# Optimization experiments

Hardware: AMD Instinct MI355X
Metric: run time of the kernel (lower is better)

## Reference

```python
import jax, jax.numpy as jnp
import numpy as np

DIM = 1024
HEADS = 16
HEAD_DIM = DIM // HEADS
EPS = 1e-6

def _layernorm(x, gamma, beta):
    # LayerNorm over last axis (head_dim), biased variance like torch
    mu = jnp.mean(x, axis=-1, keepdims=True)
    var = jnp.mean(jnp.square(x - mu), axis=-1, keepdims=True)
    return (x - mu) * jax.lax.rsqrt(var + EPS) * gamma + beta

def setup_inputs() -> dict:
    key = jax.random.key(0)
    ks = jax.random.split(key, 12)
    B, N, D = 2, 2048, DIM
    s = 1.0 / np.sqrt(D)
    inp = {
        'x': jax.random.normal(ks[0], (B, N, D), jnp.float32),
        'attn_bias': jax.random.normal(ks[1], (B, 1, N, N), jnp.float32),
        'Wq': jax.random.normal(ks[2], (D, D), jnp.float32) * s,
        'bq': jnp.zeros((D,), jnp.float32),
        'Wk': jax.random.normal(ks[3], (D, D), jnp.float32) * s,
        'bk': jnp.zeros((D,), jnp.float32),
        'Wv': jax.random.normal(ks[4], (D, D), jnp.float32) * s,
        'bv': jnp.zeros((D,), jnp.float32),
        'Wo': jax.random.normal(ks[5], (D, D), jnp.float32) * s,
        'bo': jnp.zeros((D,), jnp.float32),
        'q_gamma': jnp.ones((HEAD_DIM,), jnp.float32),
        'q_beta': jnp.zeros((HEAD_DIM,), jnp.float32),
        'k_gamma': jnp.ones((HEAD_DIM,), jnp.float32),
        'k_beta': jnp.zeros((HEAD_DIM,), jnp.float32),
    }
    return inp

def reference(x, attn_bias, Wq, bq, Wk, bk, Wv, bv, Wo, bo, q_gamma, q_beta, k_gamma, k_beta):
    B, N, D = x.shape
    h, dh = HEADS, HEAD_DIM
    # QKV projections (torch Linear: x @ W.T + b) -> (B, h, N, dh)
    def proj(W, b):
        y = jnp.einsum('bnd,ed->bne', x, W) + b
        return y.reshape(B, N, h, dh).transpose(0, 2, 1, 3)
    q = proj(Wq, bq)
    k = proj(Wk, bk)
    v = proj(Wv, bv)
    # per-head LayerNorm on Q and K
    q = _layernorm(q, q_gamma, q_beta)
    k = _layernorm(k, k_gamma, k_beta)
    # scaled dot-product attention with additive graph bias
    scores = jnp.einsum('bhnd,bhmd->bhnm', q, k) / np.sqrt(dh).astype(np.float32)
    scores = scores + attn_bias  # (B,1,N,N) broadcasts over heads
    attn = jax.nn.softmax(scores, axis=-1)
    out = jnp.einsum('bhnm,bhmd->bhnd', attn, v)
    out = out.transpose(0, 2, 1, 3).reshape(B, N, D)
    return jnp.einsum('bnd,ed->bne', out, Wo) + bo
```

## Files before the change

kernel.cpp:

```cpp
#include <hip/hip_runtime.h>
#include <hip/hip_bf16.h>
#include <hip/hip_fp16.h>

#define D_MODEL 1024
#define N_SEQ   2048
#define N_B     2
#define M_ROWS  (N_B * N_SEQ)

typedef __attribute__((ext_vector_type(8))) short bf16x8;
typedef __attribute__((ext_vector_type(4))) float f32x4;

typedef const __attribute__((address_space(1))) unsigned int gu32_t;
typedef __attribute__((address_space(3))) unsigned int lu32_t;

__device__ __forceinline__ void gload16(const void* g, void* l) {
  __builtin_amdgcn_global_load_lds((gu32_t*)g, (lu32_t*)l, 16, 0, 0);
}

__device__ inline unsigned short f2bf(float f) {
  union { float f; unsigned int u; } v; v.f = f;
  unsigned int r = (v.u + 0x7FFFu + ((v.u >> 16) & 1u)) >> 16;
  return (unsigned short)r;
}

__device__ __forceinline__ unsigned int cvt_pk_bf16(float a, float b) {
  unsigned int r;
  asm("v_cvt_pk_bf16_f32 %0, %1, %2" : "=v"(r) : "v"(a), "v"(b));
  return r;
}

__device__ __forceinline__ float exp2fast(float x) {
#if __has_builtin(__builtin_amdgcn_exp2f)
  return __builtin_amdgcn_exp2f(x);
#else
  return __expf(x * 0.69314718056f);
#endif
}

#define WAITV(N) asm volatile("s_waitcnt vmcnt(" #N ")" ::: "memory")

__device__ __forceinline__ int lds_off(int row, int col ) {
  return row * 64 + (((col >> 3) ^ (row & 7)) << 3) + (col & 7);
}

template<int ROWS, int NTHR = 256>
__device__ __forceinline__ void stage_tile(const unsigned short* gbase, size_t gstride,
                                           unsigned short* lds, int tid) {
  const int wave = tid >> 6;
#pragma unroll
  for (int rnd = 0; rnd < ROWS * 8 / NTHR; ++rnd) {
    int c = rnd * NTHR + tid;
    int row = c >> 3, pc = c & 7;
    int gcol = ((pc ^ (row & 7)) << 3);
    gload16(gbase + (size_t)row * gstride + gcol,
            lds + (size_t)(rnd * NTHR + wave * 64) * 8);
  }
}

__device__ __forceinline__ void stage_bias(const unsigned short* gbase,
                                           unsigned short* lds, int tid) {
  const int wave = tid >> 6;
#pragma unroll
  for (int rnd = 0; rnd < 2; ++rnd) {
    int c = rnd * 512 + tid;
    int row = c >> 3, pc = c & 7;
    gload16(gbase + (size_t)row * N_SEQ + pc * 8,
            lds + (size_t)(rnd * 512 + wave * 64) * 8);
  }
}

constexpr size_t XEL = (size_t)M_ROWS * D_MODEL;
constexpr size_t WEL = (size_t)D_MODEL * D_MODEL;
constexpr size_t BEL = (size_t)N_B * N_SEQ * N_SEQ;
constexpr size_t TOTEL = XEL + 4 * WEL + BEL;

__launch_bounds__(256)
__global__ void cvt_kernel(const float* __restrict__ x, const float* __restrict__ bias,
                           const float* __restrict__ wq, const float* __restrict__ wk,
                           const float* __restrict__ wv, const float* __restrict__ wo,
                           unsigned short* __restrict__ dst,
                           unsigned short* __restrict__ dstB) {
  size_t i = ((size_t)blockIdx.x * 256 + threadIdx.x) * 8;
  if (i >= TOTEL) return;
  if (i >= XEL + 4 * WEL) {
    size_t off = i - (XEL + 4 * WEL);
    int row = (int)(off >> 11);
    int key = (int)(off & 2047);
    constexpr float LOG2E = 1.44269504088896340736f;
    float4 f0 = *(const float4*)(bias + off);
    float4 f1 = *(const float4*)(bias + off + 4);
    __half t[8] = { __float2half(f0.x * LOG2E), __float2half(f0.y * LOG2E),
                    __float2half(f0.z * LOG2E), __float2half(f0.w * LOG2E),
                    __float2half(f1.x * LOG2E), __float2half(f1.y * LOG2E),
                    __float2half(f1.z * LOG2E), __float2half(f1.w * LOG2E) };
    int j  = (key >> 3) & 7;
    int jp = j ^ ((row >> 1) & 7);
    uint4 v = *(const uint4*)t;
    if (row & 1) { uint4 w; w.x = v.z; w.y = v.w; w.z = v.x; w.w = v.y; v = w; }
    *(uint4*)(dstB + (((size_t)row << 11) + (key & ~63) + jp * 8)) = v;
    return;
  }
  const float* s; size_t off = i;
  if (off < XEL)                { s = x; }
  else if (off < XEL + WEL)     { s = wq; off -= XEL; }
  else if (off < XEL + 2*WEL)   { s = wk; off -= XEL + WEL; }
  else if (off < XEL + 3*WEL)   { s = wv; off -= XEL + 2*WEL; }
  else                          { s = wo; off -= XEL + 3*WEL; }
  float4 f0 = *(const float4*)(s + off);
  float4 f1 = *(const float4*)(s + off + 4);
  unsigned short t[8] = { f2bf(f0.x), f2bf(f0.y), f2bf(f0.z), f2bf(f0.w),
                          f2bf(f1.x), f2bf(f1.y), f2bf(f1.z), f2bf(f1.w) };
  *(uint4*)(dst + i) = *(const uint4*)t;
}

__device__ __forceinline__ void mainloop128(const unsigned short* __restrict__ A,
                                            const unsigned short* __restrict__ Bw,
                                            int m0, int e0,
                                            unsigned short* As, unsigned short* Bs,
                                            f32x4 (&acc)[4][4]) {
  const int tid  = threadIdx.x;
  const int wave = tid >> 6, lane = tid & 63;
  const int l16 = lane & 15, quad = lane >> 4;
  const int wr = wave >> 1, wc = wave & 1;

  for (int kt = 0; kt < D_MODEL / 64; ++kt) {
    const int k0 = kt * 64;
    stage_tile<128>(A + (size_t)m0 * D_MODEL + k0, D_MODEL, As, tid);
    stage_tile<128>(Bw + (size_t)e0 * D_MODEL + k0, D_MODEL, Bs, tid);
    __syncthreads();
#pragma unroll
    for (int ks = 0; ks < 2; ++ks) {
      bf16x8 af[4], bfr[4];
#pragma unroll
      for (int mi = 0; mi < 4; ++mi)
        af[mi] = *(const bf16x8*)(As + lds_off(wr * 64 + mi * 16 + l16, ks * 32 + quad * 8));
#pragma unroll
      for (int ci = 0; ci < 4; ++ci)
        bfr[ci] = *(const bf16x8*)(Bs + lds_off(wc * 64 + ci * 16 + l16, ks * 32 + quad * 8));
#pragma unroll
      for (int mi = 0; mi < 4; ++mi)
#pragma unroll
        for (int ci = 0; ci < 4; ++ci)
          acc[mi][ci] = __builtin_amdgcn_mfma_f32_16x16x32_bf16(af[mi], bfr[ci], acc[mi][ci], 0, 0, 0);
    }
    __syncthreads();
  }
}

__launch_bounds__(256)
__global__ void qkv_gemm(const unsigned short* __restrict__ xb,
                         const unsigned short* __restrict__ wb,
                         const float* __restrict__ bq, const float* __restrict__ bk,
                         const float* __restrict__ bv,
                         const float* __restrict__ qg, const float* __restrict__ qbeta,
                         const float* __restrict__ kg, const float* __restrict__ kbeta,
                         unsigned short* __restrict__ qkout,
                         unsigned short* __restrict__ vt) {
  __shared__ unsigned short As[128 * 64];
  __shared__ unsigned short Bs[128 * 64];
  const int m0  = blockIdx.x * 128;
  const int by  = blockIdx.y;
  const int mat = by >> 3;
  const int e0  = (by & 7) * 128;
  const unsigned short* Bw = wb + (size_t)mat * WEL;

  f32x4 acc[4][4];
#pragma unroll
  for (int mi = 0; mi < 4; ++mi)
#pragma unroll
    for (int ci = 0; ci < 4; ++ci) acc[mi][ci] = f32x4{0.f, 0.f, 0.f, 0.f};

  mainloop128(xb, Bw, m0, e0, As, Bs, acc);

  const int lane = threadIdx.x & 63, wave = threadIdx.x >> 6;
  const int l16 = lane & 15, quad = lane >> 4;
  const int wr = wave >> 1, wc = wave & 1;
  const int colbase = e0 + wc * 64;

  const float* bias = (mat == 0) ? bq : ((mat == 1) ? bk : bv);
  float bcol[4];
#pragma unroll
  for (int ci = 0; ci < 4; ++ci) bcol[ci] = bias[colbase + ci * 16 + l16];
#pragma unroll
  for (int mi = 0; mi < 4; ++mi)
#pragma unroll
    for (int ci = 0; ci < 4; ++ci)
#pragma unroll
      for (int r = 0; r < 4; ++r) acc[mi][ci][r] += bcol[ci];

  if (mat < 2) {
    const float* gamma = (mat == 0) ? qg : kg;
    const float* beta  = (mat == 0) ? qbeta : kbeta;
    const float sc = (mat == 0) ? 0.18033688011112042f : 1.0f;
    float g4[4], bt4[4];
#pragma unroll
    for (int ci = 0; ci < 4; ++ci) {
      g4[ci] = gamma[ci * 16 + l16] * sc;
      bt4[ci] = beta[ci * 16 + l16] * sc;
    }
#pragma unroll
    for (int mi = 0; mi < 4; ++mi)
#pragma unroll
      for (int r = 0; r < 4; ++r) {
        float s = acc[mi][0][r] + acc[mi][1][r] + acc[mi][2][r] + acc[mi][3][r];
        s += __shfl_xor(s, 1); s += __shfl_xor(s, 2);
        s += __shfl_xor(s, 4); s += __shfl_xor(s, 8);
        float mean = s * (1.f / 64.f);
        float d0 = acc[mi][0][r] - mean, d1 = acc[mi][1][r] - mean;
        float d2 = acc[mi][2][r] - mean, d3 = acc[mi][3][r] - mean;
        float q = d0 * d0 + d1 * d1 + d2 * d2 + d3 * d3;
        q += __shfl_xor(q, 1); q += __shfl_xor(q, 2);
        q += __shfl_xor(q, 4); q += __shfl_xor(q, 8);
        float rs = rsqrtf(q * (1.f / 64.f) + 1e-6f);
        acc[mi][0][r] = d0 * rs * g4[0] + bt4[0];
        acc[mi][1][r] = d1 * rs * g4[1] + bt4[1];
        acc[mi][2][r] = d2 * rs * g4[2] + bt4[2];
        acc[mi][3][r] = d3 * rs * g4[3] + bt4[3];
      }
    unsigned short* out = qkout + (size_t)mat * XEL;
#pragma unroll
    for (int mi = 0; mi < 4; ++mi)
#pragma unroll
      for (int ci = 0; ci < 4; ++ci) {
        int col = colbase + ci * 16 + l16;
#pragma unroll
        for (int r = 0; r < 4; ++r) {
          int row = m0 + wr * 64 + mi * 16 + quad * 4 + r;
          out[(size_t)row * D_MODEL + col] = f2bf(acc[mi][ci][r]);
        }
      }
  } else {
    unsigned short* scr = ((wave < 2) ? As : Bs) + (size_t)(wave & 1) * 4096;
#pragma unroll
    for (int ci = 0; ci < 4; ++ci) {
      int dl = ci * 16 + l16;
      int sw = (dl & 3) * 16;
#pragma unroll
      for (int mi = 0; mi < 4; ++mi)
#pragma unroll
        for (int r = 0; r < 4; ++r) {
          int np = ((mi >> 1) << 5) + (quad << 3) + ((mi & 1) << 2) + r;
          scr[dl * 64 + (np ^ sw)] = f2bf(acc[mi][ci][r]);
        }
    }
    __builtin_amdgcn_wave_barrier();
    int row0 = m0 + wr * 64;
    int b = row0 >> 11, nb = row0 & 2047;
    int h = colbase >> 6;
    int dl = lane;
    unsigned short* gdst = vt + ((size_t)((b * 16 + h) * 64 + dl) * N_SEQ + nb);
    const unsigned short* srow = scr + dl * 64;
    int sw = (dl & 3) * 16;
#pragma unroll
    for (int j = 0; j < 8; ++j) {
      uint4 vv = *(const uint4*)(srow + ((j * 8) ^ sw));
      *(uint4*)(gdst + j * 8) = vv;
    }
  }
}

__launch_bounds__(256)
__global__ void out_gemm(const unsigned short* __restrict__ ao,
                         const unsigned short* __restrict__ wob,
                         const float* __restrict__ bo,
                         float* __restrict__ out) {
  __shared__ unsigned short As[128 * 64];
  __shared__ unsigned short Bs[128 * 64];
  const int m0 = blockIdx.x * 128;
  const int e0 = blockIdx.y * 128;

  f32x4 acc[4][4];
#pragma unroll
  for (int mi = 0; mi < 4; ++mi)
#pragma unroll
    for (int ci = 0; ci < 4; ++ci) acc[mi][ci] = f32x4{0.f, 0.f, 0.f, 0.f};

  mainloop128(ao, wob, m0, e0, As, Bs, acc);

  const int lane = threadIdx.x & 63, wave = threadIdx.x >> 6;
  const int l16 = lane & 15, quad = lane >> 4;
  const int wr = wave >> 1, wc = wave & 1;
  float bcol[4];
#pragma unroll
  for (int ci = 0; ci < 4; ++ci) bcol[ci] = bo[e0 + wc * 64 + ci * 16 + l16];
#pragma unroll
  for (int mi = 0; mi < 4; ++mi)
#pragma unroll
    for (int ci = 0; ci < 4; ++ci) {
      int col = e0 + wc * 64 + ci * 16 + l16;
#pragma unroll
      for (int r = 0; r < 4; ++r) {
        int row = m0 + wr * 64 + mi * 16 + quad * 4 + r;
        out[(size_t)row * D_MODEL + col] = acc[mi][ci][r] + bcol[ci];
      }
    }
}

__launch_bounds__(512, 4)
__global__ void attn_kernel(const unsigned short* __restrict__ Q,
                            const unsigned short* __restrict__ Kn,
                            const unsigned short* __restrict__ Vt,
                            const unsigned short* __restrict__ bias16,
                            unsigned short* __restrict__ Out) {
  __shared__ unsigned short smem[32768];

  const int tid  = threadIdx.x;
  const int wave = tid >> 6, lane = tid & 63;
  const int quad = lane >> 4, l16 = lane & 15;
  const int pairId = wave >> 1;
  const int kh = wave & 1;
  const int bidx = blockIdx.x;
  const int qt = bidx & 15;
  const int h  = (bidx >> 4) & 15;
  const int b  = bidx >> 8;
  const int q0 = qt * 128;
  const size_t base  = (size_t)b * N_SEQ * D_MODEL + (size_t)h * 64;
  const unsigned short* vtb = Vt + (size_t)(b * 16 + h) * 64 * N_SEQ;
  const unsigned short* bbase = bias16 + ((size_t)b * N_SEQ + q0) * N_SEQ;

  stage_tile<128, 512>(Q + base + (size_t)q0 * D_MODEL, D_MODEL, smem, tid);
  __syncthreads();

  bf16x8 aq[2][2];
#pragma unroll
  for (int mi = 0; mi < 2; ++mi)
#pragma unroll
    for (int ks = 0; ks < 2; ++ks)
      aq[mi][ks] = *(const bf16x8*)(smem + lds_off(pairId * 32 + mi * 16 + l16, ks * 32 + quad * 8));
  __syncthreads();

  stage_tile<64, 512>(Kn + base, D_MODEL, smem, tid);
  stage_tile<64, 512>(vtb, N_SEQ, smem + 8192, tid);
  stage_bias(bbase, smem + 16384, tid);

  WAITV(0);
  __builtin_amdgcn_s_barrier();
  __builtin_amdgcn_sched_barrier(0);

  f32x4 o[2][4];
#pragma unroll
  for (int mi = 0; mi < 2; ++mi)
#pragma unroll
    for (int cd = 0; cd < 4; ++cd) o[mi][cd] = f32x4{0.f, 0.f, 0.f, 0.f};
  float lsum[2] = {0.f, 0.f};

  constexpr int NT = N_SEQ / 64;
  for (int kt = 0; kt < NT; ++kt) {
    const int cur = kt & 1;
    unsigned short* Kcur = smem + cur * 4096;
    unsigned short* Vcur = smem + 8192 + cur * 4096;
    const unsigned short* Bcur = smem + 16384 + cur * 8192;

    if (kt + 1 < NT) {
      const int nb = cur ^ 1;
      stage_tile<64, 512>(Kn + base + (size_t)(kt + 1) * 64 * D_MODEL, D_MODEL,
                          smem + nb * 4096, tid);
      stage_tile<64, 512>(vtb + (kt + 1) * 64, N_SEQ,
                          smem + 8192 + nb * 4096, tid);
      stage_bias(bbase + (kt + 1) * 64, smem + 16384 + nb * 8192, tid);
      WAITV(4);
    } else {
      WAITV(0);
    }

    f32x4 zb[2][2];
#pragma unroll
    for (int mi = 0; mi < 2; ++mi)
#pragma unroll
      for (int cl = 0; cl < 2; ++cl) {
        uint2 bw = *(const uint2*)(Bcur + (pairId * 32 + mi * 16 + l16) * 64 +
                                   (((kh * 8 + quad + cl * 4) ^ l16) << 2));
        float2 fa = __half22float2(*(const __half2*)&bw.x);
        float2 fb = __half22float2(*(const __half2*)&bw.y);
        zb[mi][cl] = f32x4{fa.x, fa.y, fb.x, fb.y};
      }

    f32x4 sfT[2][2];
#pragma unroll
    for (int cl = 0; cl < 2; ++cl) {
      const int c = kh * 2 + cl;
      bf16x8 k0 = *(const bf16x8*)(Kcur + lds_off(c * 16 + l16, quad * 8));
      bf16x8 k1 = *(const bf16x8*)(Kcur + lds_off(c * 16 + l16, 32 + quad * 8));
      __builtin_amdgcn_s_setprio(1);
#pragma unroll
      for (int mi = 0; mi < 2; ++mi) {
        f32x4 z = __builtin_amdgcn_mfma_f32_16x16x32_bf16(k0, aq[mi][0], zb[mi][cl], 0, 0, 0);
        sfT[mi][cl] = __builtin_amdgcn_mfma_f32_16x16x32_bf16(k1, aq[mi][1], z, 0, 0, 0);
      }
      __builtin_amdgcn_s_setprio(0);
    }

    union PafU { unsigned int w[4]; bf16x8 v; };
    PafU paf[2];
#pragma unroll
    for (int mi = 0; mi < 2; ++mi)
#pragma unroll
      for (int cl = 0; cl < 2; ++cl) {
        float p0 = exp2fast(sfT[mi][cl][0]);
        float p1 = exp2fast(sfT[mi][cl][1]);
        float p2 = exp2fast(sfT[mi][cl][2]);
        float p3 = exp2fast(sfT[mi][cl][3]);
        lsum[mi] += (p0 + p1) + (p2 + p3);
        paf[mi].w[cl * 2]     = cvt_pk_bf16(p0, p1);
        paf[mi].w[cl * 2 + 1] = cvt_pk_bf16(p2, p3);
      }

    {
      bf16x8 bv[4];
#pragma unroll
      for (int cd = 0; cd < 4; ++cd)
        bv[cd] = *(const bf16x8*)(Vcur + lds_off(cd * 16 + l16, kh * 32 + quad * 8));
      __builtin_amdgcn_s_setprio(1);
#pragma unroll
      for (int mi = 0; mi < 2; ++mi)
#pragma unroll
        for (int cd = 0; cd < 4; ++cd)
          o[mi][cd] = __builtin_amdgcn_mfma_f32_16x16x32_bf16(bv[cd], paf[mi].v, o[mi][cd], 0, 0, 0);
      __builtin_amdgcn_s_setprio(0);
    }

    if (kt + 1 < NT) {
      WAITV(2);
      __builtin_amdgcn_s_barrier();
      __builtin_amdgcn_sched_barrier(0);
    }
  }

  WAITV(0);
  __syncthreads();

  float* red = (float*)smem;
  float* slot = red + (size_t)(pairId * 64 + lane) * 34;
  const int kh2 = wave & 1;
  if (kh2) {
#pragma unroll
    for (int mi = 0; mi < 2; ++mi)
#pragma unroll
      for (int cd = 0; cd < 4; ++cd)
#pragma unroll
        for (int r = 0; r < 4; ++r)
          slot[mi * 16 + cd * 4 + r] = o[mi][cd][r];
    slot[32] = lsum[0];
    slot[33] = lsum[1];
  }
  __syncthreads();
  if (!kh2) {
#pragma unroll
    for (int mi = 0; mi < 2; ++mi)
#pragma unroll
      for (int cd = 0; cd < 4; ++cd)
#pragma unroll
        for (int r = 0; r < 4; ++r)
          o[mi][cd][r] += slot[mi * 16 + cd * 4 + r];
    lsum[0] += slot[32];
    lsum[1] += slot[33];

#pragma unroll
    for (int mi = 0; mi < 2; ++mi) {
      float l = lsum[mi];
      l += __shfl_xor(l, 16);
      l += __shfl_xor(l, 32);
      float inv = 1.0f / l;
      size_t row = (size_t)b * N_SEQ + q0 + pairId * 32 + mi * 16 + l16;
#pragma unroll
      for (int cd = 0; cd < 4; ++cd) {
        uint2 vv;
        vv.x = cvt_pk_bf16(o[mi][cd][0] * inv, o[mi][cd][1] * inv);
        vv.y = cvt_pk_bf16(o[mi][cd][2] * inv, o[mi][cd][3] * inv);
        *(uint2*)(Out + row * D_MODEL + h * 64 + cd * 16 + quad * 4) = vv;
      }
    }
  }
}

extern "C" void kernel_launch(void* const* d_in, const int* in_sizes, int n_in,
                              void* d_out, int out_size, void* d_ws, size_t ws_size,
                              hipStream_t stream) {
  const float* x    = (const float*)d_in[0];
  const float* bias = (const float*)d_in[1];
  const float* Wq = (const float*)d_in[2];  const float* bq = (const float*)d_in[3];
  const float* Wk = (const float*)d_in[4];  const float* bk = (const float*)d_in[5];
  const float* Wv = (const float*)d_in[6];  const float* bv = (const float*)d_in[7];
  const float* Wo = (const float*)d_in[8];  const float* bo = (const float*)d_in[9];
  const float* qg = (const float*)d_in[10]; const float* qb = (const float*)d_in[11];
  const float* kg = (const float*)d_in[12]; const float* kb = (const float*)d_in[13];
  float* out = (float*)d_out;

  unsigned short* wsb = (unsigned short*)d_ws;
  unsigned short* xb  = wsb;
  unsigned short* wqb = wsb + XEL;
  unsigned short* wob = wsb + XEL + 3 * WEL;
  unsigned short* qn  = wsb + XEL + 4 * WEL;
  unsigned short* kn  = qn + XEL;
  unsigned short* vt  = qn + 2 * XEL;
  unsigned short* b16 = qn + 3 * XEL;
  unsigned short* ao  = xb;

  dim3 blk(256, 1, 1);

  cvt_kernel<<<dim3((unsigned)(TOTEL / (256 * 8)), 1, 1), blk, 0, stream>>>(
      x, bias, Wq, Wk, Wv, Wo, wsb, b16);

  qkv_gemm<<<dim3(M_ROWS / 128, 24, 1), blk, 0, stream>>>(
      xb, wqb, bq, bk, bv, qg, qb, kg, kb, qn, vt);

  attn_kernel<<<dim3(N_B * 16 * (N_SEQ / 128), 1, 1), dim3(512, 1, 1), 0, stream>>>(
      qn, kn, vt, b16, ao);

  out_gemm<<<dim3(M_ROWS / 128, D_MODEL / 128, 1), blk, 0, stream>>>(ao, wob, bo, out);
}
```

Before: 234.9 us.

## Triple-buffer K tiles with two-ahead prefetch and remap block order

The attention kernel now keeps three K tile buffers in LDS and prefetches K two iterations ahead, while V and bias stay double-buffered one iteration ahead. The wait counts are rebalanced, and the mid-loop wait before the barrier is dropped. The aim is to hide more global load latency behind the MFMA work. The block index is also permuted so that consecutive blocks span different batch, head and query tile groups, which changes cache locality across CUs. LDS use grows from 64KB to 72KB per block, which may reduce occupancy.

```diff
diff --git a/kernel.cpp b/kernel.cpp
--- a/kernel.cpp
+++ b/kernel.cpp
@@ -302,14 +302,15 @@
                             const unsigned short* __restrict__ Vt,
                             const unsigned short* __restrict__ bias16,
                             unsigned short* __restrict__ Out) {
-  __shared__ unsigned short smem[32768];
+  __shared__ unsigned short smem[36864];
 
   const int tid  = threadIdx.x;
   const int wave = tid >> 6, lane = tid & 63;
   const int quad = lane >> 4, l16 = lane & 15;
   const int pairId = wave >> 1;
   const int kh = wave & 1;
-  const int bidx = blockIdx.x;
+  const int bidx0 = blockIdx.x;
+  const int bidx = (bidx0 & 7) * 64 + (bidx0 >> 3);
   const int qt = bidx & 15;
   const int h  = (bidx >> 4) & 15;
   const int b  = bidx >> 8;
@@ -330,10 +331,12 @@
   __syncthreads();
 
   stage_tile<64, 512>(Kn + base, D_MODEL, smem, tid);
-  stage_tile<64, 512>(vtb, N_SEQ, smem + 8192, tid);
-  stage_bias(bbase, smem + 16384, tid);
-
-  WAITV(0);
+  stage_tile<64, 512>(vtb, N_SEQ, smem + 12288, tid);
+  stage_bias(bbase, smem + 20480, tid);
+  stage_tile<64, 512>(Kn + base + (size_t)64 * D_MODEL, D_MODEL,
+                      smem + 4096, tid);
+
+  WAITV(1);
   __builtin_amdgcn_s_barrier();
   __builtin_amdgcn_sched_barrier(0);
 
@@ -346,22 +349,21 @@
 
   constexpr int NT = N_SEQ / 64;
   for (int kt = 0; kt < NT; ++kt) {
-    const int cur = kt & 1;
-    unsigned short* Kcur = smem + cur * 4096;
-    unsigned short* Vcur = smem + 8192 + cur * 4096;
-    const unsigned short* Bcur = smem + 16384 + cur * 8192;
-
+    unsigned short* Kcur = smem + (kt % 3) * 4096;
+    unsigned short* Vcur = smem + 12288 + (kt & 1) * 4096;
+    const unsigned short* Bcur = smem + 20480 + (kt & 1) * 8192;
+
+    if (kt + 2 < NT)
+      stage_tile<64, 512>(Kn + base + (size_t)(kt + 2) * 64 * D_MODEL, D_MODEL,
+                          smem + ((kt + 2) % 3) * 4096, tid);
     if (kt + 1 < NT) {
-      const int nb = cur ^ 1;
-      stage_tile<64, 512>(Kn + base + (size_t)(kt + 1) * 64 * D_MODEL, D_MODEL,
-                          smem + nb * 4096, tid);
       stage_tile<64, 512>(vtb + (kt + 1) * 64, N_SEQ,
-                          smem + 8192 + nb * 4096, tid);
-      stage_bias(bbase + (kt + 1) * 64, smem + 16384 + nb * 8192, tid);
-      WAITV(4);
-    } else {
-      WAITV(0);
-    }
+                          smem + 12288 + ((kt + 1) & 1) * 4096, tid);
+      stage_bias(bbase + (kt + 1) * 64, smem + 20480 + ((kt + 1) & 1) * 8192, tid);
+    }
+    if (kt < NT - 2)      { WAITV(4); }
+    else if (kt == NT - 2){ WAITV(3); }
+    else                  { WAITV(0); }
 
     f32x4 zb[2][2];
 #pragma unroll
@@ -420,7 +422,6 @@
     }
 
     if (kt + 1 < NT) {
-      WAITV(2);
       __builtin_amdgcn_s_barrier();
       __builtin_amdgcn_sched_barrier(0);
     }
@@ -431,8 +432,7 @@
 
   float* red = (float*)smem;
   float* slot = red + (size_t)(pairId * 64 + lane) * 34;
-  const int kh2 = wave & 1;
-  if (kh2) {
+  if (kh) {
 #pragma unroll
     for (int mi = 0; mi < 2; ++mi)
 #pragma unroll
@@ -444,7 +444,7 @@
     slot[33] = lsum[1];
   }
   __syncthreads();
-  if (!kh2) {
+  if (!kh) {
 #pragma unroll
     for (int mi = 0; mi < 2; ++mi)
 #pragma unroll
```

Result: no change. 232.9 us (-0.8%).
